# Performance work log

Measured on AMD Instinct MI355X. Metric: run time of the kernel, lower is better.

The kernel has to match this reference:

```python
import jax, jax.numpy as jnp
from jax import lax
import numpy as np

I, H, C = 128, 512, 1000  # input_dim, hidden_dim, num_classes
B, S = 256, 512           # batch, seq_len


def setup_inputs() -> dict:
    key = jax.random.key(0)
    ks = jax.random.split(key, 7)
    k = 1.0 / np.sqrt(H)  # pytorch GRU/Linear init range
    return {
        "x": jax.random.normal(ks[0], (B, S, I), dtype=jnp.float32),
        "W_ih": jax.random.uniform(ks[1], (3 * H, I), minval=-k, maxval=k, dtype=jnp.float32),
        "W_hh": jax.random.uniform(ks[2], (3 * H, H), minval=-k, maxval=k, dtype=jnp.float32),
        "b_ih": jax.random.uniform(ks[3], (3 * H,), minval=-k, maxval=k, dtype=jnp.float32),
        "b_hh": jax.random.uniform(ks[4], (3 * H,), minval=-k, maxval=k, dtype=jnp.float32),
        "W_head": jax.random.uniform(ks[5], (C, H), minval=-k, maxval=k, dtype=jnp.float32),
        "b_head": jax.random.uniform(ks[6], (C,), minval=-k, maxval=k, dtype=jnp.float32),
    }


def reference(x, W_ih, W_hh, b_ih, b_hh, W_head, b_head):
    # Precompute input projections for all timesteps: [B,S,3H] -> [S,B,3H]
    x_gates = jnp.einsum("bsi,gi->bsg", x, W_ih) + b_ih
    x_gates = jnp.transpose(x_gates, (1, 0, 2))

    h0 = jnp.zeros((x.shape[0], W_hh.shape[1]), dtype=x.dtype)

    def step(h, xg):
        hg = h @ W_hh.T + b_hh  # [B,3H]
        xr, xz, xn = jnp.split(xg, 3, axis=-1)
        hr, hz, hn = jnp.split(hg, 3, axis=-1)
        r = jax.nn.sigmoid(xr + hr)
        z = jax.nn.sigmoid(xz + hz)
        n = jnp.tanh(xn + r * hn)
        h_new = (1.0 - z) * n + z * h
        return h_new, None

    hT, _ = lax.scan(step, h0, x_gates)  # final hidden state == outputs[:, -1, :]
    return hT @ W_head.T + b_head  # [B, C]
```

## Files before the change

### kernel.cpp

```cpp
#include <hip/hip_runtime.h>


#define NB 256
#define NH 512
#define NI 128
#define NC 1000
#define NS 512

typedef __attribute__((ext_vector_type(8))) short bf16x8;
typedef __attribute__((ext_vector_type(4))) float f32x4;

__device__ __forceinline__ unsigned short f2bf(float f) {
    unsigned u = __builtin_bit_cast(unsigned, f);
    return (unsigned short)((u + 0x7FFFu + ((u >> 16) & 1u)) >> 16);
}

__device__ __forceinline__ bf16x8 pack8(const float* v) {
    bf16x8 r;
#pragma unroll
    for (int i = 0; i < 8; ++i) r[i] = (short)f2bf(v[i]);
    return r;
}

__device__ __forceinline__ unsigned long long ld_agent_u64(const unsigned long long* p) {
    return __hip_atomic_load(p, __ATOMIC_RELAXED, __HIP_MEMORY_SCOPE_AGENT);
}
__device__ __forceinline__ void st_agent_u16(unsigned short* p, unsigned short v) {
    __hip_atomic_store(p, v, __ATOMIC_RELAXED, __HIP_MEMORY_SCOPE_AGENT);
}

__global__ void gru_init_ws(unsigned long long* __restrict__ hb,
                            unsigned long long* __restrict__ cn) {
    const int i = blockIdx.x * 256 + threadIdx.x;
    if (i < 32768)
        __hip_atomic_store(hb + i, 0ull, __ATOMIC_RELAXED, __HIP_MEMORY_SCOPE_AGENT);
    else if (i < 32768 + 4096)
        __hip_atomic_store(cn + (i - 32768), 0ull, __ATOMIC_RELAXED, __HIP_MEMORY_SCOPE_AGENT);
}

__global__ void __launch_bounds__(256, 1) gru_scan(
    const float* __restrict__ x,
    const float* __restrict__ Wih,
    const float* __restrict__ Whh,
    const float* __restrict__ bih,
    const float* __restrict__ bhh,
    unsigned short* __restrict__ hbuf,
    float* __restrict__ hT,
    unsigned int* __restrict__ cnt)
{
    const int tid = threadIdx.x;
    const int l   = tid & 63;
    const int w   = tid >> 6;
    const int ch  = w & 1;
    const int kh  = w >> 1;
    const int bid = blockIdx.x;
    const int g   = bid & 15;
    const int jb  = bid >> 4;
    const int r0  = g << 4;
    const int cw0 = (jb << 5) + (ch << 4);
    const int l15 = l & 15;
    const int lq  = l >> 4;

    __shared__ float part[4][6][64][4];

    bf16x8 whh[3][8];
#pragma unroll
    for (int nt = 0; nt < 3; ++nt) {
        const int jr = nt * NH + cw0 + l15;
        const float* wr = Whh + jr * NH;
#pragma unroll
        for (int ks = 0; ks < 8; ++ks) {
            const int k0 = kh * 256 + ks * 32 + lq * 8;
            float tmp[8];
            *(f32x4*)(tmp)     = *(const f32x4*)(wr + k0);
            *(f32x4*)(tmp + 4) = *(const f32x4*)(wr + k0 + 4);
            whh[nt][ks] = pack8(tmp);
        }
    }
    bf16x8 wih[3][2];
#pragma unroll
    for (int nt = 0; nt < 3; ++nt) {
        const int jr = nt * NH + cw0 + l15;
        const float* wr = Wih + jr * NI;
#pragma unroll
        for (int ks = 0; ks < 2; ++ks) {
            const int k0 = kh * 64 + ks * 32 + lq * 8;
            float tmp[8];
            *(f32x4*)(tmp)     = *(const f32x4*)(wr + k0);
            *(f32x4*)(tmp + 4) = *(const f32x4*)(wr + k0 + 4);
            wih[nt][ks] = pack8(tmp);
        }
    }

    const int c_col = cw0 + l15;
    float bi0 = bih[c_col], bi1 = bih[NH + c_col], bi2 = bih[2 * NH + c_col];
    float bh0 = bhh[c_col], bh1 = bhh[NH + c_col], bh2 = bhh[2 * NH + c_col];
    if (kh != 0) { bi0 = bi1 = bi2 = bh0 = bh1 = bh2 = 0.f; }

    float hold0 = 0.f, hold1 = 0.f;

    const int arow = r0 + l15;
    const int aoff = arow * NH + kh * 256 + lq * 8;
    const float* xptr0 = x + arow * (NS * NI) + kh * 64 + lq * 8;

    f32x4 xp0 = *(const f32x4*)(xptr0 + 0);
    f32x4 xp1 = *(const f32x4*)(xptr0 + 4);
    f32x4 xp2 = *(const f32x4*)(xptr0 + 32);
    f32x4 xp3 = *(const f32x4*)(xptr0 + 36);

    unsigned int* cg = cnt + (g << 9);

    for (int t = 0; t < NS; ++t) {
        const int cur = t & 1;
        const unsigned short* hr_ = hbuf + cur * (NB * NH);
        unsigned short* hw_ = hbuf + (cur ^ 1) * (NB * NH);

        const unsigned long long* hq = (const unsigned long long*)(hr_ + aoff);
        bf16x8 afr[8];
#pragma unroll
        for (int ks = 0; ks < 8; ++ks) {
            union { unsigned long long q[2]; bf16x8 v; } u;
            u.q[0] = ld_agent_u64(hq + ks * 8 + 0);
            u.q[1] = ld_agent_u64(hq + ks * 8 + 1);
            afr[ks] = u.v;
        }

        f32x4 hg0 = {bh0, bh0, bh0, bh0}, hg1 = {bh1, bh1, bh1, bh1}, hg2 = {bh2, bh2, bh2, bh2};
        f32x4 xg0 = {bi0, bi0, bi0, bi0}, xg1 = {bi1, bi1, bi1, bi1}, xg2 = {bi2, bi2, bi2, bi2};

        {
            float xt[16];
            *(f32x4*)(xt)      = xp0; *(f32x4*)(xt + 4)  = xp1;
            *(f32x4*)(xt + 8)  = xp2; *(f32x4*)(xt + 12) = xp3;
            bf16x8 xf0 = pack8(xt), xf1 = pack8(xt + 8);
            xg0 = __builtin_amdgcn_mfma_f32_16x16x32_bf16(xf0, wih[0][0], xg0, 0, 0, 0);
            xg1 = __builtin_amdgcn_mfma_f32_16x16x32_bf16(xf0, wih[1][0], xg1, 0, 0, 0);
            xg2 = __builtin_amdgcn_mfma_f32_16x16x32_bf16(xf0, wih[2][0], xg2, 0, 0, 0);
            xg0 = __builtin_amdgcn_mfma_f32_16x16x32_bf16(xf1, wih[0][1], xg0, 0, 0, 0);
            xg1 = __builtin_amdgcn_mfma_f32_16x16x32_bf16(xf1, wih[1][1], xg1, 0, 0, 0);
            xg2 = __builtin_amdgcn_mfma_f32_16x16x32_bf16(xf1, wih[2][1], xg2, 0, 0, 0);
        }

#pragma unroll
        for (int ks = 0; ks < 8; ++ks) {
            hg0 = __builtin_amdgcn_mfma_f32_16x16x32_bf16(afr[ks], whh[0][ks], hg0, 0, 0, 0);
            hg1 = __builtin_amdgcn_mfma_f32_16x16x32_bf16(afr[ks], whh[1][ks], hg1, 0, 0, 0);
            hg2 = __builtin_amdgcn_mfma_f32_16x16x32_bf16(afr[ks], whh[2][ks], hg2, 0, 0, 0);
        }

        if (t + 1 < NS) {
            const float* xp = xptr0 + (t + 1) * NI;
            xp0 = *(const f32x4*)(xp + 0);
            xp1 = *(const f32x4*)(xp + 4);
            xp2 = *(const f32x4*)(xp + 32);
            xp3 = *(const f32x4*)(xp + 36);
        }

        *(f32x4*)&part[w][0][l][0] = hg0;
        *(f32x4*)&part[w][1][l][0] = hg1;
        *(f32x4*)&part[w][2][l][0] = hg2;
        *(f32x4*)&part[w][3][l][0] = xg0;
        *(f32x4*)&part[w][4][l][0] = xg1;
        *(f32x4*)&part[w][5][l][0] = xg2;
        __syncthreads();
        const int pw = w ^ 2;
        const f32x4 ph0 = *(const f32x4*)&part[pw][0][l][0];
        const f32x4 ph1 = *(const f32x4*)&part[pw][1][l][0];
        const f32x4 ph2 = *(const f32x4*)&part[pw][2][l][0];
        const f32x4 px0 = *(const f32x4*)&part[pw][3][l][0];
        const f32x4 px1 = *(const f32x4*)&part[pw][4][l][0];
        const f32x4 px2 = *(const f32x4*)&part[pw][5][l][0];

        float vh0[2], vh1[2], vh2[2], vx0[2], vx1[2], vx2[2];
        if (kh == 0) {
            vh0[0] = hg0[0] + ph0[0]; vh0[1] = hg0[1] + ph0[1];
            vh1[0] = hg1[0] + ph1[0]; vh1[1] = hg1[1] + ph1[1];
            vh2[0] = hg2[0] + ph2[0]; vh2[1] = hg2[1] + ph2[1];
            vx0[0] = xg0[0] + px0[0]; vx0[1] = xg0[1] + px0[1];
            vx1[0] = xg1[0] + px1[0]; vx1[1] = xg1[1] + px1[1];
            vx2[0] = xg2[0] + px2[0]; vx2[1] = xg2[1] + px2[1];
        } else {
            vh0[0] = hg0[2] + ph0[2]; vh0[1] = hg0[3] + ph0[3];
            vh1[0] = hg1[2] + ph1[2]; vh1[1] = hg1[3] + ph1[3];
            vh2[0] = hg2[2] + ph2[2]; vh2[1] = hg2[3] + ph2[3];
            vx0[0] = xg0[2] + px0[2]; vx0[1] = xg0[3] + px0[3];
            vx1[0] = xg1[2] + px1[2]; vx1[1] = xg1[3] + px1[3];
            vx2[0] = xg2[2] + px2[2]; vx2[1] = xg2[3] + px2[3];
        }

#pragma unroll
        for (int q = 0; q < 2; ++q) {
            const float rr = __builtin_amdgcn_rcpf(1.f + __expf(-(vx0[q] + vh0[q])));
            const float zz = __builtin_amdgcn_rcpf(1.f + __expf(-(vx1[q] + vh1[q])));
            const float a  = vx2[q] + rr * vh2[q];
            const float e2 = __expf(2.f * a);
            const float nn = (e2 - 1.f) * __builtin_amdgcn_rcpf(e2 + 1.f);
            const float hp = q ? hold1 : hold0;
            const float hnew = (1.f - zz) * nn + zz * hp;
            if (q) hold1 = hnew; else hold0 = hnew;
            const int row = r0 + lq * 4 + (kh * 2 + q);
            st_agent_u16(hw_ + row * NH + c_col, f2bf(hnew));
            if (t == NS - 1) hT[row * NH + c_col] = hnew;
        }

        if (t < NS - 1) {
            __syncthreads();
            if (tid == 0) {
                __hip_atomic_fetch_add(cg + t, 1u, __ATOMIC_RELAXED, __HIP_MEMORY_SCOPE_AGENT);
                while (__hip_atomic_load(cg + t, __ATOMIC_RELAXED, __HIP_MEMORY_SCOPE_AGENT) < 16u) {}
            }
            __syncthreads();
        }
    }
}

__global__ void __launch_bounds__(256, 1) gru_head(
    const float* __restrict__ hT,
    const float* __restrict__ Wh,
    const float* __restrict__ bh,
    float* __restrict__ out)
{
    __shared__ float hs[16 * 512];
    const int tid = threadIdx.x;
    const int rg  = blockIdx.x;
    const int cgp = blockIdx.y;
    const float* src = hT + rg * (16 * 512);
#pragma unroll
    for (int i = 0; i < 32; ++i) hs[tid + 256 * i] = src[tid + 256 * i];
    __syncthreads();
    const int col = (cgp << 6) + (tid & 63);
    const int rb  = (tid >> 6) << 2;
    if (col < NC) {
        const float* wr = Wh + col * NH;
        float a0 = 0.f, a1 = 0.f, a2 = 0.f, a3 = 0.f;
        for (int k = 0; k < NH; k += 4) {
            const f32x4 wv = *(const f32x4*)(wr + k);
            const f32x4 h0 = *(const f32x4*)&hs[(rb + 0) * NH + k];
            const f32x4 h1 = *(const f32x4*)&hs[(rb + 1) * NH + k];
            const f32x4 h2 = *(const f32x4*)&hs[(rb + 2) * NH + k];
            const f32x4 h3 = *(const f32x4*)&hs[(rb + 3) * NH + k];
#pragma unroll
            for (int j = 0; j < 4; ++j) {
                a0 = fmaf(wv[j], h0[j], a0);
                a1 = fmaf(wv[j], h1[j], a1);
                a2 = fmaf(wv[j], h2[j], a2);
                a3 = fmaf(wv[j], h3[j], a3);
            }
        }
        const float bb = bh[col];
        const int orow = (rg << 4) + rb;
        out[(orow + 0) * NC + col] = a0 + bb;
        out[(orow + 1) * NC + col] = a1 + bb;
        out[(orow + 2) * NC + col] = a2 + bb;
        out[(orow + 3) * NC + col] = a3 + bb;
    }
}

extern "C" void kernel_launch(void* const* d_in, const int* in_sizes, int n_in,
                              void* d_out, int out_size, void* d_ws, size_t ws_size,
                              hipStream_t stream)
{
    (void)in_sizes; (void)n_in; (void)out_size; (void)ws_size;
    const float* x     = (const float*)d_in[0];
    const float* Wih   = (const float*)d_in[1];
    const float* Whh   = (const float*)d_in[2];
    const float* bih   = (const float*)d_in[3];
    const float* bhh   = (const float*)d_in[4];
    const float* Whead = (const float*)d_in[5];
    const float* bhead = (const float*)d_in[6];
    float* out = (float*)d_out;

    char* ws = (char*)d_ws;
    unsigned short* hbuf = (unsigned short*)ws;
    unsigned int*   cnt  = (unsigned int*)(ws + 2 * NB * NH * 2);
    float*          hT   = (float*)(ws + 2 * NB * NH * 2 + 16 * NS * 4);

    gru_init_ws<<<144, 256, 0, stream>>>((unsigned long long*)hbuf, (unsigned long long*)cnt);
    gru_scan<<<256, 256, 0, stream>>>(x, Wih, Whh, bih, bhh, hbuf, hT, cnt);
    gru_head<<<dim3(16, 16), 256, 0, stream>>>(hT, Whead, bhead, out);
}
```

Before: 1.732 ms.

## Replace per-step counter barrier with per-block flags and full-K waves

Halves the persistent grid to 128 blocks, each covering 64 hidden columns, and gives each wave the full K=512 reduction. This removes the cross-wave split-K reduction through shared memory. The per-step atomic counter barrier is replaced by per-producer flags that consumers poll with a wave vote. Hidden state is written in a blocked layout that is staged into LDS and shared across waves. Each wave now holds twice as many weight registers, which risks register pressure. Flag polling by every wave also adds memory traffic.

```diff
diff --git a/kernel.cpp b/kernel.cpp
--- a/kernel.cpp
+++ b/kernel.cpp
@@ -25,17 +25,19 @@
 __device__ __forceinline__ unsigned long long ld_agent_u64(const unsigned long long* p) {
     return __hip_atomic_load(p, __ATOMIC_RELAXED, __HIP_MEMORY_SCOPE_AGENT);
 }
+__device__ __forceinline__ unsigned int ld_agent_u32(const unsigned int* p) {
+    return __hip_atomic_load(p, __ATOMIC_RELAXED, __HIP_MEMORY_SCOPE_AGENT);
+}
 __device__ __forceinline__ void st_agent_u16(unsigned short* p, unsigned short v) {
     __hip_atomic_store(p, v, __ATOMIC_RELAXED, __HIP_MEMORY_SCOPE_AGENT);
 }
-
-__global__ void gru_init_ws(unsigned long long* __restrict__ hb,
-                            unsigned long long* __restrict__ cn) {
+__device__ __forceinline__ void st_agent_u32(unsigned int* p, unsigned int v) {
+    __hip_atomic_store(p, v, __ATOMIC_RELAXED, __HIP_MEMORY_SCOPE_AGENT);
+}
+
+__global__ void gru_init_ws(unsigned int* __restrict__ fl) {
     const int i = blockIdx.x * 256 + threadIdx.x;
-    if (i < 32768)
-        __hip_atomic_store(hb + i, 0ull, __ATOMIC_RELAXED, __HIP_MEMORY_SCOPE_AGENT);
-    else if (i < 32768 + 4096)
-        __hip_atomic_store(cn + (i - 32768), 0ull, __ATOMIC_RELAXED, __HIP_MEMORY_SCOPE_AGENT);
+    if (i < 512) fl[i] = 0u;
 }
 
 __global__ void __launch_bounds__(256, 1) gru_scan(
@@ -46,170 +48,146 @@
     const float* __restrict__ bhh,
     unsigned short* __restrict__ hbuf,
     float* __restrict__ hT,
-    unsigned int* __restrict__ cnt)
+    unsigned int* __restrict__ flags)
 {
     const int tid = threadIdx.x;
     const int l   = tid & 63;
     const int w   = tid >> 6;
-    const int ch  = w & 1;
-    const int kh  = w >> 1;
+    const int l15 = l & 15;
+    const int lq  = l >> 4;
     const int bid = blockIdx.x;
     const int g   = bid & 15;
     const int jb  = bid >> 4;
-    const int r0  = g << 4;
-    const int cw0 = (jb << 5) + (ch << 4);
-    const int l15 = l & 15;
-    const int lq  = l >> 4;
-
-    __shared__ float part[4][6][64][4];
-
-    bf16x8 whh[3][8];
-#pragma unroll
-    for (int nt = 0; nt < 3; ++nt) {
-        const int jr = nt * NH + cw0 + l15;
-        const float* wr = Whh + jr * NH;
-#pragma unroll
-        for (int ks = 0; ks < 8; ++ks) {
-            const int k0 = kh * 256 + ks * 32 + lq * 8;
+    const int c   = jb * 64 + w * 16 + l15;
+
+    __shared__ __align__(16) unsigned short hstage[16 * 512];
+
+    bf16x8 whh[3][16];
+#pragma unroll
+    for (int gt = 0; gt < 3; ++gt) {
+        const float* wr = Whh + (size_t)(gt * NH + c) * NH;
+#pragma unroll
+        for (int ks = 0; ks < 16; ++ks) {
             float tmp[8];
-            *(f32x4*)(tmp)     = *(const f32x4*)(wr + k0);
-            *(f32x4*)(tmp + 4) = *(const f32x4*)(wr + k0 + 4);
-            whh[nt][ks] = pack8(tmp);
-        }
-    }
-    bf16x8 wih[3][2];
-#pragma unroll
-    for (int nt = 0; nt < 3; ++nt) {
-        const int jr = nt * NH + cw0 + l15;
-        const float* wr = Wih + jr * NI;
-#pragma unroll
-        for (int ks = 0; ks < 2; ++ks) {
-            const int k0 = kh * 64 + ks * 32 + lq * 8;
+            *(f32x4*)(tmp)     = *(const f32x4*)(wr + ks * 32 + lq * 8);
+            *(f32x4*)(tmp + 4) = *(const f32x4*)(wr + ks * 32 + lq * 8 + 4);
+            whh[gt][ks] = pack8(tmp);
+        }
+    }
+    bf16x8 wih[3][4];
+#pragma unroll
+    for (int gt = 0; gt < 3; ++gt) {
+        const float* wr = Wih + (size_t)(gt * NH + c) * NI;
+#pragma unroll
+        for (int ks = 0; ks < 4; ++ks) {
             float tmp[8];
-            *(f32x4*)(tmp)     = *(const f32x4*)(wr + k0);
-            *(f32x4*)(tmp + 4) = *(const f32x4*)(wr + k0 + 4);
-            wih[nt][ks] = pack8(tmp);
-        }
-    }
-
-    const int c_col = cw0 + l15;
-    float bi0 = bih[c_col], bi1 = bih[NH + c_col], bi2 = bih[2 * NH + c_col];
-    float bh0 = bhh[c_col], bh1 = bhh[NH + c_col], bh2 = bhh[2 * NH + c_col];
-    if (kh != 0) { bi0 = bi1 = bi2 = bh0 = bh1 = bh2 = 0.f; }
-
-    float hold0 = 0.f, hold1 = 0.f;
-
-    const int arow = r0 + l15;
-    const int aoff = arow * NH + kh * 256 + lq * 8;
-    const float* xptr0 = x + arow * (NS * NI) + kh * 64 + lq * 8;
-
-    f32x4 xp0 = *(const f32x4*)(xptr0 + 0);
-    f32x4 xp1 = *(const f32x4*)(xptr0 + 4);
-    f32x4 xp2 = *(const f32x4*)(xptr0 + 32);
-    f32x4 xp3 = *(const f32x4*)(xptr0 + 36);
-
-    unsigned int* cg = cnt + (g << 9);
+            *(f32x4*)(tmp)     = *(const f32x4*)(wr + ks * 32 + lq * 8);
+            *(f32x4*)(tmp + 4) = *(const f32x4*)(wr + ks * 32 + lq * 8 + 4);
+            wih[gt][ks] = pack8(tmp);
+        }
+    }
+
+    const float bR = bih[c] + bhh[c];
+    const float bZ = bih[NH + c] + bhh[NH + c];
+    const float bNx = bih[2 * NH + c];
+    const float bNh = bhh[2 * NH + c];
+
+    float hprev[4] = {0.f, 0.f, 0.f, 0.f};
+
+    const float* xrow = x + (size_t)(g * 16 + l15) * (NS * NI) + lq * 8;
+    unsigned int* fl = flags + g * 32;
+
+    const int Fst   = jb * 2 + (w >> 1);
+    const int lanep = ((w & 1) * 2 + (l15 >> 3)) * 16;
+    const int est   = l15 & 7;
 
     for (int t = 0; t < NS; ++t) {
-        const int cur = t & 1;
-        const unsigned short* hr_ = hbuf + cur * (NB * NH);
-        unsigned short* hw_ = hbuf + (cur ^ 1) * (NB * NH);
-
-        const unsigned long long* hq = (const unsigned long long*)(hr_ + aoff);
-        bf16x8 afr[8];
-#pragma unroll
-        for (int ks = 0; ks < 8; ++ks) {
-            union { unsigned long long q[2]; bf16x8 v; } u;
-            u.q[0] = ld_agent_u64(hq + ks * 8 + 0);
-            u.q[1] = ld_agent_u64(hq + ks * 8 + 1);
-            afr[ks] = u.v;
-        }
-
-        f32x4 hg0 = {bh0, bh0, bh0, bh0}, hg1 = {bh1, bh1, bh1, bh1}, hg2 = {bh2, bh2, bh2, bh2};
-        f32x4 xg0 = {bi0, bi0, bi0, bi0}, xg1 = {bi1, bi1, bi1, bi1}, xg2 = {bi2, bi2, bi2, bi2};
-
+        const int rb = t & 1, wb = rb ^ 1;
+
+        if (t > 0) {
+            unsigned int myf;
+            do { myf = ld_agent_u32(fl + (l & 7)); }
+            while (!__all((int)(myf >= (unsigned)t)));
+            __builtin_amdgcn_sched_barrier(0);
+            asm volatile("" ::: "memory");
+
+            unsigned long long q0[4], q1[4];
+#pragma unroll
+            for (int j = 0; j < 4; ++j) {
+                const int f = w * 4 + j;
+                const unsigned long long* p =
+                    (const unsigned long long*)(hbuf + (((size_t)rb * 16 + g) * 16 + f) * 512) + (l << 1);
+                q0[j] = ld_agent_u64(p);
+                q1[j] = ld_agent_u64(p + 1);
+            }
+#pragma unroll
+            for (int j = 0; j < 4; ++j) {
+                const int f = w * 4 + j;
+                union { unsigned long long q[2]; bf16x8 v; } u;
+                u.q[0] = q0[j]; u.q[1] = q1[j];
+                *(bf16x8*)&hstage[f * 512 + l * 8] = u.v;
+            }
+        }
+
+        bf16x8 xf[4];
         {
-            float xt[16];
-            *(f32x4*)(xt)      = xp0; *(f32x4*)(xt + 4)  = xp1;
-            *(f32x4*)(xt + 8)  = xp2; *(f32x4*)(xt + 12) = xp3;
-            bf16x8 xf0 = pack8(xt), xf1 = pack8(xt + 8);
-            xg0 = __builtin_amdgcn_mfma_f32_16x16x32_bf16(xf0, wih[0][0], xg0, 0, 0, 0);
-            xg1 = __builtin_amdgcn_mfma_f32_16x16x32_bf16(xf0, wih[1][0], xg1, 0, 0, 0);
-            xg2 = __builtin_amdgcn_mfma_f32_16x16x32_bf16(xf0, wih[2][0], xg2, 0, 0, 0);
-            xg0 = __builtin_amdgcn_mfma_f32_16x16x32_bf16(xf1, wih[0][1], xg0, 0, 0, 0);
-            xg1 = __builtin_amdgcn_mfma_f32_16x16x32_bf16(xf1, wih[1][1], xg1, 0, 0, 0);
-            xg2 = __builtin_amdgcn_mfma_f32_16x16x32_bf16(xf1, wih[2][1], xg2, 0, 0, 0);
-        }
-
-#pragma unroll
-        for (int ks = 0; ks < 8; ++ks) {
-            hg0 = __builtin_amdgcn_mfma_f32_16x16x32_bf16(afr[ks], whh[0][ks], hg0, 0, 0, 0);
-            hg1 = __builtin_amdgcn_mfma_f32_16x16x32_bf16(afr[ks], whh[1][ks], hg1, 0, 0, 0);
-            hg2 = __builtin_amdgcn_mfma_f32_16x16x32_bf16(afr[ks], whh[2][ks], hg2, 0, 0, 0);
-        }
-
-        if (t + 1 < NS) {
-            const float* xp = xptr0 + (t + 1) * NI;
-            xp0 = *(const f32x4*)(xp + 0);
-            xp1 = *(const f32x4*)(xp + 4);
-            xp2 = *(const f32x4*)(xp + 32);
-            xp3 = *(const f32x4*)(xp + 36);
-        }
-
-        *(f32x4*)&part[w][0][l][0] = hg0;
-        *(f32x4*)&part[w][1][l][0] = hg1;
-        *(f32x4*)&part[w][2][l][0] = hg2;
-        *(f32x4*)&part[w][3][l][0] = xg0;
-        *(f32x4*)&part[w][4][l][0] = xg1;
-        *(f32x4*)&part[w][5][l][0] = xg2;
-        __syncthreads();
-        const int pw = w ^ 2;
-        const f32x4 ph0 = *(const f32x4*)&part[pw][0][l][0];
-        const f32x4 ph1 = *(const f32x4*)&part[pw][1][l][0];
-        const f32x4 ph2 = *(const f32x4*)&part[pw][2][l][0];
-        const f32x4 px0 = *(const f32x4*)&part[pw][3][l][0];
-        const f32x4 px1 = *(const f32x4*)&part[pw][4][l][0];
-        const f32x4 px2 = *(const f32x4*)&part[pw][5][l][0];
-
-        float vh0[2], vh1[2], vh2[2], vx0[2], vx1[2], vx2[2];
-        if (kh == 0) {
-            vh0[0] = hg0[0] + ph0[0]; vh0[1] = hg0[1] + ph0[1];
-            vh1[0] = hg1[0] + ph1[0]; vh1[1] = hg1[1] + ph1[1];
-            vh2[0] = hg2[0] + ph2[0]; vh2[1] = hg2[1] + ph2[1];
-            vx0[0] = xg0[0] + px0[0]; vx0[1] = xg0[1] + px0[1];
-            vx1[0] = xg1[0] + px1[0]; vx1[1] = xg1[1] + px1[1];
-            vx2[0] = xg2[0] + px2[0]; vx2[1] = xg2[1] + px2[1];
-        } else {
-            vh0[0] = hg0[2] + ph0[2]; vh0[1] = hg0[3] + ph0[3];
-            vh1[0] = hg1[2] + ph1[2]; vh1[1] = hg1[3] + ph1[3];
-            vh2[0] = hg2[2] + ph2[2]; vh2[1] = hg2[3] + ph2[3];
-            vx0[0] = xg0[2] + px0[2]; vx0[1] = xg0[3] + px0[3];
-            vx1[0] = xg1[2] + px1[2]; vx1[1] = xg1[3] + px1[3];
-            vx2[0] = xg2[2] + px2[2]; vx2[1] = xg2[3] + px2[3];
-        }
-
-#pragma unroll
-        for (int q = 0; q < 2; ++q) {
-            const float rr = __builtin_amdgcn_rcpf(1.f + __expf(-(vx0[q] + vh0[q])));
-            const float zz = __builtin_amdgcn_rcpf(1.f + __expf(-(vx1[q] + vh1[q])));
-            const float a  = vx2[q] + rr * vh2[q];
+            const float* xt = xrow + t * NI;
+#pragma unroll
+            for (int ks = 0; ks < 4; ++ks) {
+                float tmp[8];
+                *(f32x4*)(tmp)     = *(const f32x4*)(xt + ks * 32);
+                *(f32x4*)(tmp + 4) = *(const f32x4*)(xt + ks * 32 + 4);
+                xf[ks] = pack8(tmp);
+            }
+        }
+        f32x4 aR  = {bR, bR, bR, bR};
+        f32x4 aZ  = {bZ, bZ, bZ, bZ};
+        f32x4 aNx = {bNx, bNx, bNx, bNx};
+        f32x4 aNh = {bNh, bNh, bNh, bNh};
+#pragma unroll
+        for (int ks = 0; ks < 4; ++ks) {
+            aR  = __builtin_amdgcn_mfma_f32_16x16x32_bf16(xf[ks], wih[0][ks], aR, 0, 0, 0);
+            aZ  = __builtin_amdgcn_mfma_f32_16x16x32_bf16(xf[ks], wih[1][ks], aZ, 0, 0, 0);
+            aNx = __builtin_amdgcn_mfma_f32_16x16x32_bf16(xf[ks], wih[2][ks], aNx, 0, 0, 0);
+        }
+
+        if (t > 0) {
+            __syncthreads();
+#pragma unroll
+            for (int ks = 0; ks < 16; ++ks) {
+                const bf16x8 af = *(const bf16x8*)&hstage[ks * 512 + l * 8];
+                aR  = __builtin_amdgcn_mfma_f32_16x16x32_bf16(af, whh[0][ks], aR, 0, 0, 0);
+                aZ  = __builtin_amdgcn_mfma_f32_16x16x32_bf16(af, whh[1][ks], aZ, 0, 0, 0);
+                aNh = __builtin_amdgcn_mfma_f32_16x16x32_bf16(af, whh[2][ks], aNh, 0, 0, 0);
+            }
+        }
+
+        float hnew[4];
+#pragma unroll
+        for (int i = 0; i < 4; ++i) {
+            const float rr = __builtin_amdgcn_rcpf(1.f + __expf(-aR[i]));
+            const float zz = __builtin_amdgcn_rcpf(1.f + __expf(-aZ[i]));
+            const float a  = aNx[i] + rr * aNh[i];
             const float e2 = __expf(2.f * a);
             const float nn = (e2 - 1.f) * __builtin_amdgcn_rcpf(e2 + 1.f);
-            const float hp = q ? hold1 : hold0;
-            const float hnew = (1.f - zz) * nn + zz * hp;
-            if (q) hold1 = hnew; else hold0 = hnew;
-            const int row = r0 + lq * 4 + (kh * 2 + q);
-            st_agent_u16(hw_ + row * NH + c_col, f2bf(hnew));
-            if (t == NS - 1) hT[row * NH + c_col] = hnew;
+            hnew[i] = (1.f - zz) * nn + zz * hprev[i];
+            hprev[i] = hnew[i];
         }
 
         if (t < NS - 1) {
+            unsigned short* dst = hbuf + (((size_t)wb * 16 + g) * 16 + Fst) * 512;
+#pragma unroll
+            for (int i = 0; i < 4; ++i) {
+                const int rl = lq * 4 + i;
+                st_agent_u16(dst + (lanep + rl) * 8 + est, f2bf(hnew[i]));
+            }
+            asm volatile("s_waitcnt vmcnt(0)" ::: "memory");
             __syncthreads();
-            if (tid == 0) {
-                __hip_atomic_fetch_add(cg + t, 1u, __ATOMIC_RELAXED, __HIP_MEMORY_SCOPE_AGENT);
-                while (__hip_atomic_load(cg + t, __ATOMIC_RELAXED, __HIP_MEMORY_SCOPE_AGENT) < 16u) {}
-            }
-            __syncthreads();
+            if (tid == 0) st_agent_u32(&fl[jb], (unsigned)(t + 1));
+        } else {
+#pragma unroll
+            for (int i = 0; i < 4; ++i)
+                hT[(size_t)(g * 16 + lq * 4 + i) * NH + c] = hnew[i];
         }
     }
 }
@@ -271,11 +249,11 @@
     float* out = (float*)d_out;
 
     char* ws = (char*)d_ws;
-    unsigned short* hbuf = (unsigned short*)ws;
-    unsigned int*   cnt  = (unsigned int*)(ws + 2 * NB * NH * 2);
-    float*          hT   = (float*)(ws + 2 * NB * NH * 2 + 16 * NS * 4);
-
-    gru_init_ws<<<144, 256, 0, stream>>>((unsigned long long*)hbuf, (unsigned long long*)cnt);
-    gru_scan<<<256, 256, 0, stream>>>(x, Wih, Whh, bih, bhh, hbuf, hT, cnt);
+    unsigned short* hbuf  = (unsigned short*)ws;
+    unsigned int*   flags = (unsigned int*)(ws + 512 * 1024);
+    float*          hT    = (float*)(ws + 512 * 1024 + 2048);
+
+    gru_init_ws<<<2, 256, 0, stream>>>(flags);
+    gru_scan<<<128, 256, 0, stream>>>(x, Wih, Whh, bih, bhh, hbuf, hT, flags);
     gru_head<<<dim3(16, 16), 256, 0, stream>>>(hT, Whead, bhead, out);
 }
```

Measured after the change: 2.562 ms. +48.0%, slower.
